# Kernel tuning notes

Measured on AMD Instinct MI355X. Metric: run time of the kernel, lower is better.

Reference implementation:

```python
import jax, jax.numpy as jnp
import numpy as np


def setup_inputs() -> dict:
    key = jax.random.key(0)
    kq, kk, kv = jax.random.split(key, 3)
    B, S, H, D = 2, 2048, 32, 128
    q = jax.random.normal(kq, (B, S, H, D), dtype=jnp.float32)
    k = jax.random.normal(kk, (B, S, H, D), dtype=jnp.float32)
    v = jax.random.normal(kv, (B, S, H, D), dtype=jnp.float32)
    return {"q": q, "k": k, "v": v}


def _causal_attention(q, k, v):
    # q,k,v: [B, S, H, D] (flash-attn layout). Zigzag ring attention computes
    # exactly standard causal attention; zigzag only balances work across ranks.
    B, S, H, D = q.shape
    scale = 1.0 / jnp.sqrt(jnp.asarray(D, q.dtype))
    scores = jnp.einsum('bqhd,bkhd->bhqk', q, k) * scale  # [B,H,S,S]
    causal = jnp.tril(jnp.ones((S, S), dtype=bool))
    scores = jnp.where(causal, scores, jnp.finfo(scores.dtype).min)
    probs = jax.nn.softmax(scores, axis=-1)
    return jnp.einsum('bhqk,bkhd->bqhd', probs, v)  # [B,S,H,D]


def reference(q, k, v):
    out = _causal_attention(q, k, v)
    return jnp.sum(out)
```

## Files before the change

### kernel.cpp

```cpp
#include <hip/hip_runtime.h>
#include <hip/hip_bf16.h>
#include <stdint.h>

#define B_ 2
#define S_ 2048
#define H_ 32
#define D_ 128
#define R_ (B_*H_*S_)
#define PG 2048
#define VSU (B_ * S_)
#define CPB 40

typedef __bf16 bf16x8 __attribute__((ext_vector_type(8)));
typedef float  f32x16 __attribute__((ext_vector_type(16)));

#if __has_builtin(__builtin_amdgcn_exp2f)
#define EXP2F(x) __builtin_amdgcn_exp2f(x)
#else
#define EXP2F(x) exp2f(x)
#endif

#define AS1 __attribute__((address_space(1)))
#define AS3 __attribute__((address_space(3)))

__device__ __forceinline__ unsigned short f2bf(float f) {
  unsigned u = __float_as_uint(f);
  u += 0x7FFFu + ((u >> 16) & 1u);
  return (unsigned short)(u >> 16);
}

__global__ __launch_bounds__(256) void prep(
    const float* __restrict__ k, const float* __restrict__ v,
    unsigned short* __restrict__ kb,
    float* __restrict__ vsum, float* __restrict__ nd, float* __restrict__ out0) {
  const int bid = blockIdx.x;
  const int t = threadIdx.x;
  if (bid == 0 && t == 0) out0[0] = 0.f;

  #pragma unroll
  for (int g = 0; g < (R_ * D_ / 8) / (PG * 256); ++g) {
    const size_t i = (size_t)g * (PG * 256) + bid * 256 + t;
    const float4 a = *reinterpret_cast<const float4*>(k + i * 8);
    const float4 b = *reinterpret_cast<const float4*>(k + i * 8 + 4);
    ushort4 o0, o1;
    o0.x = f2bf(a.x); o0.y = f2bf(a.y); o0.z = f2bf(a.z); o0.w = f2bf(a.w);
    o1.x = f2bf(b.x); o1.y = f2bf(b.y); o1.z = f2bf(b.z); o1.w = f2bf(b.w);
    *reinterpret_cast<ushort4*>(kb + i * 8)     = o0;
    *reinterpret_cast<ushort4*>(kb + i * 8 + 4) = o1;
  }

  #pragma unroll
  for (int g = 0; g < VSU / PG; ++g) {
    const int u = bid + g * PG;
    const int b = u / S_, s = u % S_;
    const int h = t >> 3, i = t & 7;
    const float* p = v + (((size_t)b * S_ + s) * H_ + h) * D_ + i * 16;
    const float4 a0 = *reinterpret_cast<const float4*>(p + 0);
    const float4 a1 = *reinterpret_cast<const float4*>(p + 4);
    const float4 a2 = *reinterpret_cast<const float4*>(p + 8);
    const float4 a3 = *reinterpret_cast<const float4*>(p + 12);
    float sum = (a0.x+a0.y+a0.z+a0.w) + (a1.x+a1.y+a1.z+a1.w)
              + (a2.x+a2.y+a2.z+a2.w) + (a3.x+a3.y+a3.z+a3.w);
    sum += __shfl_xor(sum, 1);
    sum += __shfl_xor(sum, 2);
    sum += __shfl_xor(sum, 4);
    if (i == 0) vsum[((size_t)b * H_ + h) * S_ + s] = sum;
  }

  if (bid < 256) {
    float4* p = reinterpret_cast<float4*>(nd);
    p[(size_t)bid * 256 + t] = float4{0.f, 0.f, 0.f, 0.f};
  }
}

__global__ __launch_bounds__(256, 4) void attn_sum(
    const float* __restrict__ qf_, const unsigned short* __restrict__ kb_,
    const float* __restrict__ vsum, float* __restrict__ numb,
    float* __restrict__ denb) {
  __shared__ uint4 kbuf[4][512];
  __shared__ float vsbuf[4][64];

  const int id = blockIdx.x;
  const int y  = id >> 3;
  const int bh = (id & 7) + 8 * (y / CPB);
  const int c  = y % CPB;

  int qt, h, nch;
  if (c < 4)       { qt = c;                 h = 0;            nch = 1; }
  else if (c < 12) { qt = 4 + ((c - 4) >> 1);  h = (c - 4) & 1;  nch = 2; }
  else if (c < 24) { qt = 8 + (c - 12) / 3;    h = (c - 12) % 3; nch = 3; }
  else             { qt = 12 + ((c - 24) >> 2); h = (c - 24) & 3; nch = 4; }
  const int nkt  = 2 * qt + 2;
  const int bas_ = nkt / nch, rem = nkt % nch;
  const int kt0  = h * bas_ + (h < rem ? h : rem);
  const int kt1  = kt0 + bas_ + (h < rem ? 1 : 0);
  const int st0  = 2 * kt0, st1 = 2 * kt1;

  const int t  = threadIdx.x;
  const int w  = t >> 6;
  const int l  = t & 63;
  const int ln = l & 31, l5 = l >> 5;

  const int b0 = bh >> 5, h0 = bh & 31;
  const int qrow0 = qt * 128 + w * 32;
  const unsigned short* ksrc0 = kb_ + ((size_t)b0 * S_ * H_ + h0) * D_;
  const float* vsrc0 = vsum + (size_t)bh * S_;

  const float sc = 0.0883883476483184f * 1.4426950408889634f;
  bf16x8 qfrag[8];
  {
    const float* qp = qf_ + (((size_t)b0 * S_ + qrow0 + ln) * H_ + h0) * D_ + l5 * 8;
    #pragma unroll
    for (int kb8 = 0; kb8 < 8; ++kb8) {
      const float4 a = *reinterpret_cast<const float4*>(qp + kb8 * 16);
      const float4 b = *reinterpret_cast<const float4*>(qp + kb8 * 16 + 4);
      union { unsigned short u[8]; bf16x8 v; } uu;
      uu.u[0] = f2bf(a.x * sc); uu.u[1] = f2bf(a.y * sc);
      uu.u[2] = f2bf(a.z * sc); uu.u[3] = f2bf(a.w * sc);
      uu.u[4] = f2bf(b.x * sc); uu.u[5] = f2bf(b.y * sc);
      uu.u[6] = f2bf(b.z * sc); uu.u[7] = f2bf(b.w * sc);
      qfrag[kb8] = uu.v;
    }
  }

  auto stage = [&](int st, int slot) {
    #pragma unroll
    for (int j = 0; j < 2; ++j) {
      const int idx = (w * 2 + j) * 64 + l;
      const int r   = idx >> 4;
      const int p   = idx & 15;
      const int cc  = p ^ (r & 15);
      const unsigned short* src = ksrc0 + (size_t)(st * 32 + r) * (H_ * D_) + cc * 8;
      __builtin_amdgcn_global_load_lds(
          (const AS1 void*)src, (AS3 void*)(&kbuf[slot][idx & ~63]), 16, 0, 0);
    }
    __builtin_amdgcn_global_load_lds(
        (const AS1 void*)(vsrc0 + st * 32 + l), (AS3 void*)(&vsbuf[slot][0]), 4, 0, 0);
  };

  float num[16], den[16];
  #pragma unroll
  for (int r = 0; r < 16; ++r) { num[r] = 0.f; den[r] = 0.f; }

  stage(st0, st0 & 3);
  stage(st0 + 1, (st0 + 1) & 3);

  const int xr = ln & 15;
  for (int st = st0; st < st1; ++st) {
    if (st + 1 < st1) asm volatile("s_waitcnt vmcnt(3)" ::: "memory");
    else              asm volatile("s_waitcnt vmcnt(0)" ::: "memory");
    __builtin_amdgcn_s_barrier();
    if (st + 2 < st1) stage(st + 2, (st + 2) & 3);

    const int kbase = st * 32;
    if (kbase <= qrow0 + 31) {
      const int slot = st & 3;
      const uint4* rowb = &kbuf[slot][ln * 16];
      f32x16 sacc = {0.f,0.f,0.f,0.f,0.f,0.f,0.f,0.f,
                     0.f,0.f,0.f,0.f,0.f,0.f,0.f,0.f};
      __builtin_amdgcn_s_setprio(1);
      #pragma unroll
      for (int kb8 = 0; kb8 < 8; ++kb8) {
        const bf16x8 bf = *reinterpret_cast<const bf16x8*>(&rowb[(kb8 * 2 + l5) ^ xr]);
        sacc = __builtin_amdgcn_mfma_f32_32x32x16_bf16(qfrag[kb8], bf, sacc, 0, 0, 0);
      }
      __builtin_amdgcn_s_setprio(0);
      const float vsv = vsbuf[slot][ln];
      if (kbase + 31 <= qrow0) {
        #pragma unroll
        for (int r = 0; r < 16; ++r) {
          const float e = EXP2F(sacc[r]);
          den[r] += e;
          num[r] = fmaf(e, vsv, num[r]);
        }
      } else {
        const int kgc = kbase + ln;
        #pragma unroll
        for (int r = 0; r < 16; ++r) {
          const int qgr = qrow0 + (r & 3) + 8 * (r >> 2) + 4 * l5;
          const float e = (kgc <= qgr) ? EXP2F(sacc[r]) : 0.f;
          den[r] += e;
          num[r] = fmaf(e, vsv, num[r]);
        }
      }
    }
  }

  #pragma unroll
  for (int m = 1; m < 32; m <<= 1) {
    #pragma unroll
    for (int r = 0; r < 16; ++r) {
      num[r] += __shfl_xor(num[r], m);
      den[r] += __shfl_xor(den[r], m);
    }
  }
  if (ln == 0) {
    float* nrow = numb + (size_t)bh * S_;
    float* drow = denb + (size_t)bh * S_;
    #pragma unroll
    for (int r = 0; r < 16; ++r) {
      const int qgr = qrow0 + (r & 3) + 8 * (r >> 2) + 4 * l5;
      atomicAdd(&nrow[qgr], num[r]);
      atomicAdd(&drow[qgr], den[r]);
    }
  }
}

__global__ __launch_bounds__(256) void finalize(
    const float* __restrict__ numb, const float* __restrict__ denb,
    float* __restrict__ out) {
  const int i = blockIdx.x * 256 + threadIdx.x;
  float c = numb[i] / denb[i];
  #pragma unroll
  for (int m = 1; m < 64; m <<= 1) c += __shfl_xor(c, m);
  __shared__ float ps[4];
  if ((threadIdx.x & 63) == 0) ps[threadIdx.x >> 6] = c;
  __syncthreads();
  if (threadIdx.x == 0) atomicAdd(out, ps[0] + ps[1] + ps[2] + ps[3]);
}

extern "C" void kernel_launch(void* const* d_in, const int* in_sizes, int n_in,
                              void* d_out, int out_size, void* d_ws, size_t ws_size,
                              hipStream_t stream) {
  const float* q = (const float*)d_in[0];
  const float* k = (const float*)d_in[1];
  const float* v = (const float*)d_in[2];
  float* out = (float*)d_out;

  unsigned short* kb = (unsigned short*)d_ws;
  float* vsum = (float*)(kb + (size_t)R_ * D_);
  float* numb = vsum + R_;
  float* denb = numb + R_;

  hipLaunchKernelGGL(prep, dim3(PG), dim3(256), 0, stream,
                     k, v, kb, vsum, numb, out);
  hipLaunchKernelGGL(attn_sum, dim3(64 * CPB), dim3(256), 0, stream,
                     q, kb, vsum, numb, denb);
  hipLaunchKernelGGL(finalize, dim3(R_ / 256), dim3(256), 0, stream,
                     numb, denb, out);
}
```

Baseline: 111.5 us.

## Precast Q to bf16 in prep and stage K via registers with software pipeline

The prep kernel now also converts Q to scaled bf16, so the attention kernel loads ready-made bf16 Q fragments instead of converting fp32 Q per block. K staging replaces direct global-to-LDS loads with register loads double-buffered two steps ahead, then swizzled ds_writes to LDS, with adjusted waitcnt accounting. This cuts redundant Q conversion and fp32 Q traffic in the hot kernel. In exchange it adds an extra Q write and read pass in prep plus more register pressure and LDS write instructions in the loop.

Result: slower. 142.0 us (+27.4%).

```diff
diff --git a/kernel.cpp b/kernel.cpp
--- a/kernel.cpp
+++ b/kernel.cpp
@@ -8,7 +8,6 @@
 #define D_ 128
 #define R_ (B_*H_*S_)
 #define PG 2048
-#define VSU (B_ * S_)
 #define CPB 40
 
 typedef __bf16 bf16x8 __attribute__((ext_vector_type(8)));
@@ -30,27 +29,32 @@
 }
 
 __global__ __launch_bounds__(256) void prep(
-    const float* __restrict__ k, const float* __restrict__ v,
-    unsigned short* __restrict__ kb,
+    const float* __restrict__ qf, const float* __restrict__ kf,
+    const float* __restrict__ v,
+    unsigned short* __restrict__ qc, unsigned short* __restrict__ kc,
     float* __restrict__ vsum, float* __restrict__ nd, float* __restrict__ out0) {
   const int bid = blockIdx.x;
   const int t = threadIdx.x;
   if (bid == 0 && t == 0) out0[0] = 0.f;
 
   #pragma unroll
-  for (int g = 0; g < (R_ * D_ / 8) / (PG * 256); ++g) {
-    const size_t i = (size_t)g * (PG * 256) + bid * 256 + t;
-    const float4 a = *reinterpret_cast<const float4*>(k + i * 8);
-    const float4 b = *reinterpret_cast<const float4*>(k + i * 8 + 4);
-    ushort4 o0, o1;
-    o0.x = f2bf(a.x); o0.y = f2bf(a.y); o0.z = f2bf(a.z); o0.w = f2bf(a.w);
-    o1.x = f2bf(b.x); o1.y = f2bf(b.y); o1.z = f2bf(b.z); o1.w = f2bf(b.w);
-    *reinterpret_cast<ushort4*>(kb + i * 8)     = o0;
-    *reinterpret_cast<ushort4*>(kb + i * 8 + 4) = o1;
-  }
-
-  #pragma unroll
-  for (int g = 0; g < VSU / PG; ++g) {
+  for (int g = 0; g < 8; ++g) {
+    const size_t i = (size_t)g * (PG * 256) + (size_t)bid * 256 + t;
+    const float* src; unsigned short* dst; float sc;
+    if (g < 4) { src = qf; dst = qc; sc = 0.0883883476483184f * 1.4426950408889634f; }
+    else       { src = kf - (size_t)R_ * D_; dst = kc - (size_t)R_ * D_; sc = 1.0f; }
+    const float4 a = *reinterpret_cast<const float4*>(src + i * 8);
+    const float4 b = *reinterpret_cast<const float4*>(src + i * 8 + 4);
+    union { unsigned short u[8]; uint4 v4; } o;
+    o.u[0] = f2bf(a.x * sc); o.u[1] = f2bf(a.y * sc);
+    o.u[2] = f2bf(a.z * sc); o.u[3] = f2bf(a.w * sc);
+    o.u[4] = f2bf(b.x * sc); o.u[5] = f2bf(b.y * sc);
+    o.u[6] = f2bf(b.z * sc); o.u[7] = f2bf(b.w * sc);
+    *reinterpret_cast<uint4*>(dst + i * 8) = o.v4;
+  }
+
+  #pragma unroll
+  for (int g = 0; g < (B_ * S_) / PG; ++g) {
     const int u = bid + g * PG;
     const int b = u / S_, s = u % S_;
     const int h = t >> 3, i = t & 7;
@@ -74,7 +78,7 @@
 }
 
 __global__ __launch_bounds__(256, 4) void attn_sum(
-    const float* __restrict__ qf_, const unsigned short* __restrict__ kb_,
+    const unsigned short* __restrict__ qc, const unsigned short* __restrict__ kc,
     const float* __restrict__ vsum, float* __restrict__ numb,
     float* __restrict__ denb) {
   __shared__ uint4 kbuf[4][512];
@@ -103,54 +107,67 @@
 
   const int b0 = bh >> 5, h0 = bh & 31;
   const int qrow0 = qt * 128 + w * 32;
-  const unsigned short* ksrc0 = kb_ + ((size_t)b0 * S_ * H_ + h0) * D_;
+  const unsigned short* kc0 = kc + ((size_t)b0 * S_ * H_ + h0) * D_;
   const float* vsrc0 = vsum + (size_t)bh * S_;
 
-  const float sc = 0.0883883476483184f * 1.4426950408889634f;
   bf16x8 qfrag[8];
   {
-    const float* qp = qf_ + (((size_t)b0 * S_ + qrow0 + ln) * H_ + h0) * D_ + l5 * 8;
+    const unsigned short* qp =
+        qc + (((size_t)b0 * S_ + qrow0 + ln) * H_ + h0) * D_ + l5 * 8;
     #pragma unroll
-    for (int kb8 = 0; kb8 < 8; ++kb8) {
-      const float4 a = *reinterpret_cast<const float4*>(qp + kb8 * 16);
-      const float4 b = *reinterpret_cast<const float4*>(qp + kb8 * 16 + 4);
-      union { unsigned short u[8]; bf16x8 v; } uu;
-      uu.u[0] = f2bf(a.x * sc); uu.u[1] = f2bf(a.y * sc);
-      uu.u[2] = f2bf(a.z * sc); uu.u[3] = f2bf(a.w * sc);
-      uu.u[4] = f2bf(b.x * sc); uu.u[5] = f2bf(b.y * sc);
-      uu.u[6] = f2bf(b.z * sc); uu.u[7] = f2bf(b.w * sc);
-      qfrag[kb8] = uu.v;
-    }
-  }
-
-  auto stage = [&](int st, int slot) {
-    #pragma unroll
-    for (int j = 0; j < 2; ++j) {
-      const int idx = (w * 2 + j) * 64 + l;
-      const int r   = idx >> 4;
-      const int p   = idx & 15;
-      const int cc  = p ^ (r & 15);
-      const unsigned short* src = ksrc0 + (size_t)(st * 32 + r) * (H_ * D_) + cc * 8;
-      __builtin_amdgcn_global_load_lds(
-          (const AS1 void*)src, (AS3 void*)(&kbuf[slot][idx & ~63]), 16, 0, 0);
-    }
+    for (int kb8 = 0; kb8 < 8; ++kb8)
+      qfrag[kb8] = *reinterpret_cast<const bf16x8*>(qp + kb8 * 16);
+  }
+
+  const int rloc = w * 8 + (l >> 3);
+  const int cc1  = (l & 7) * 2;
+  const int xrw  = rloc & 15;
+
+  auto LOADK = [&](int st, uint4& r0, uint4& r1) {
+    const unsigned short* p = kc0 + (size_t)(st * 32 + rloc) * (H_ * D_) + cc1 * 8;
+    r0 = *reinterpret_cast<const uint4*>(p);
+    r1 = *reinterpret_cast<const uint4*>(p + 8);
+  };
+  auto DSW = [&](int slot, uint4 r0, uint4 r1) {
+    kbuf[slot][rloc * 16 + (cc1 ^ xrw)]       = r0;
+    kbuf[slot][rloc * 16 + ((cc1 + 1) ^ xrw)] = r1;
+  };
+  auto VSD = [&](int st) {
     __builtin_amdgcn_global_load_lds(
-        (const AS1 void*)(vsrc0 + st * 32 + l), (AS3 void*)(&vsbuf[slot][0]), 4, 0, 0);
+        (const AS1 void*)(vsrc0 + st * 32 + l),
+        (AS3 void*)(&vsbuf[st & 3][0]), 4, 0, 0);
   };
 
   float num[16], den[16];
   #pragma unroll
   for (int r = 0; r < 16; ++r) { num[r] = 0.f; den[r] = 0.f; }
 
-  stage(st0, st0 & 3);
-  stage(st0 + 1, (st0 + 1) & 3);
+  uint4 a0, a1, b0r, b1r;
+
+  if ((st0 & 1) == 0) LOADK(st0, a0, a1); else LOADK(st0, b0r, b1r);
+  VSD(st0);
+  if (st0 + 1 < st1) {
+    if (((st0 + 1) & 1) == 0) LOADK(st0 + 1, a0, a1); else LOADK(st0 + 1, b0r, b1r);
+    VSD(st0 + 1);
+  }
+  if ((st0 & 1) == 0) DSW(st0 & 3, a0, a1); else DSW(st0 & 3, b0r, b1r);
 
   const int xr = ln & 15;
   for (int st = st0; st < st1; ++st) {
-    if (st + 1 < st1) asm volatile("s_waitcnt vmcnt(3)" ::: "memory");
-    else              asm volatile("s_waitcnt vmcnt(0)" ::: "memory");
+    asm volatile("s_waitcnt lgkmcnt(0)" ::: "memory");
     __builtin_amdgcn_s_barrier();
-    if (st + 2 < st1) stage(st + 2, (st + 2) & 3);
+    if (st + 1 < st1) {
+      if (((st + 1) & 1) == 0) DSW((st + 1) & 3, a0, a1);
+      else                     DSW((st + 1) & 3, b0r, b1r);
+    }
+    if (st + 2 < st1) {
+      if (((st + 2) & 1) == 0) LOADK(st + 2, a0, a1);
+      else                     LOADK(st + 2, b0r, b1r);
+      VSD(st + 2);
+    }
+    if (st + 2 < st1)      asm volatile("s_waitcnt vmcnt(6)" ::: "memory");
+    else if (st + 1 < st1) asm volatile("s_waitcnt vmcnt(3)" ::: "memory");
+    else                   asm volatile("s_waitcnt vmcnt(0)" ::: "memory");
 
     const int kbase = st * 32;
     if (kbase <= qrow0 + 31) {
@@ -227,15 +244,16 @@
   const float* v = (const float*)d_in[2];
   float* out = (float*)d_out;
 
-  unsigned short* kb = (unsigned short*)d_ws;
-  float* vsum = (float*)(kb + (size_t)R_ * D_);
+  unsigned short* qc = (unsigned short*)d_ws;
+  unsigned short* kc = qc + (size_t)R_ * D_;
+  float* vsum = (float*)(kc + (size_t)R_ * D_);
   float* numb = vsum + R_;
   float* denb = numb + R_;
 
   hipLaunchKernelGGL(prep, dim3(PG), dim3(256), 0, stream,
-                     k, v, kb, vsum, numb, out);
+                     q, k, v, qc, kc, vsum, numb, out);
   hipLaunchKernelGGL(attn_sum, dim3(64 * CPB), dim3(256), 0, stream,
-                     q, kb, vsum, numb, denb);
+                     qc, kc, vsum, numb, denb);
   hipLaunchKernelGGL(finalize, dim3(R_ / 256), dim3(256), 0, stream,
                      numb, denb, out);
 }
```

## Fuse K bf16 conversion into attention via register-staged pipeline

Applied to the files above, without the earlier changes.

Removes the separate K fp32-to-bf16 conversion pass from the prep kernel. The attention kernel now loads fp32 K tiles into registers, keeping three stages in flight, and converts them with packed bf16 conversion instructions. It then writes them into swizzled LDS, replacing the async global-to-LDS loads. This saves a full write and reread of a bf16 K copy, but each tile now reads twice as many bytes of fp32 K, register pressure rises, and occupancy drops to 3 blocks per SIMD.

After: 233.3 us. 109% more time.

```diff
diff --git a/kernel.cpp b/kernel.cpp
--- a/kernel.cpp
+++ b/kernel.cpp
@@ -8,7 +8,6 @@
 #define D_ 128
 #define R_ (B_*H_*S_)
 #define PG 2048
-#define VSU (B_ * S_)
 #define CPB 40
 
 typedef __bf16 bf16x8 __attribute__((ext_vector_type(8)));
@@ -23,34 +22,21 @@
 #define AS1 __attribute__((address_space(1)))
 #define AS3 __attribute__((address_space(3)))
 
-__device__ __forceinline__ unsigned short f2bf(float f) {
-  unsigned u = __float_as_uint(f);
-  u += 0x7FFFu + ((u >> 16) & 1u);
-  return (unsigned short)(u >> 16);
+__device__ __forceinline__ unsigned int cvtpk(float a, float b) {
+  unsigned int r;
+  asm volatile("v_cvt_pk_bf16_f32 %0, %1, %2" : "=v"(r) : "v"(a), "v"(b));
+  return r;
 }
 
 __global__ __launch_bounds__(256) void prep(
-    const float* __restrict__ k, const float* __restrict__ v,
-    unsigned short* __restrict__ kb,
-    float* __restrict__ vsum, float* __restrict__ nd, float* __restrict__ out0) {
+    const float* __restrict__ v, float* __restrict__ vsum,
+    float* __restrict__ nd, float* __restrict__ out0) {
   const int bid = blockIdx.x;
   const int t = threadIdx.x;
   if (bid == 0 && t == 0) out0[0] = 0.f;
 
   #pragma unroll
-  for (int g = 0; g < (R_ * D_ / 8) / (PG * 256); ++g) {
-    const size_t i = (size_t)g * (PG * 256) + bid * 256 + t;
-    const float4 a = *reinterpret_cast<const float4*>(k + i * 8);
-    const float4 b = *reinterpret_cast<const float4*>(k + i * 8 + 4);
-    ushort4 o0, o1;
-    o0.x = f2bf(a.x); o0.y = f2bf(a.y); o0.z = f2bf(a.z); o0.w = f2bf(a.w);
-    o1.x = f2bf(b.x); o1.y = f2bf(b.y); o1.z = f2bf(b.z); o1.w = f2bf(b.w);
-    *reinterpret_cast<ushort4*>(kb + i * 8)     = o0;
-    *reinterpret_cast<ushort4*>(kb + i * 8 + 4) = o1;
-  }
-
-  #pragma unroll
-  for (int g = 0; g < VSU / PG; ++g) {
+  for (int g = 0; g < (B_ * S_) / PG; ++g) {
     const int u = bid + g * PG;
     const int b = u / S_, s = u % S_;
     const int h = t >> 3, i = t & 7;
@@ -73,8 +59,8 @@
   }
 }
 
-__global__ __launch_bounds__(256, 4) void attn_sum(
-    const float* __restrict__ qf_, const unsigned short* __restrict__ kb_,
+__global__ __launch_bounds__(256, 3) void attn_sum(
+    const float* __restrict__ qf, const float* __restrict__ kf,
     const float* __restrict__ vsum, float* __restrict__ numb,
     float* __restrict__ denb) {
   __shared__ uint4 kbuf[4][512];
@@ -103,54 +89,81 @@
 
   const int b0 = bh >> 5, h0 = bh & 31;
   const int qrow0 = qt * 128 + w * 32;
-  const unsigned short* ksrc0 = kb_ + ((size_t)b0 * S_ * H_ + h0) * D_;
+  const float* kf0 = kf + ((size_t)b0 * S_ * H_ + h0) * D_;
   const float* vsrc0 = vsum + (size_t)bh * S_;
 
   const float sc = 0.0883883476483184f * 1.4426950408889634f;
   bf16x8 qfrag[8];
   {
-    const float* qp = qf_ + (((size_t)b0 * S_ + qrow0 + ln) * H_ + h0) * D_ + l5 * 8;
+    const float* qp = qf + (((size_t)b0 * S_ + qrow0 + ln) * H_ + h0) * D_ + l5 * 8;
     #pragma unroll
     for (int kb8 = 0; kb8 < 8; ++kb8) {
       const float4 a = *reinterpret_cast<const float4*>(qp + kb8 * 16);
       const float4 b = *reinterpret_cast<const float4*>(qp + kb8 * 16 + 4);
-      union { unsigned short u[8]; bf16x8 v; } uu;
-      uu.u[0] = f2bf(a.x * sc); uu.u[1] = f2bf(a.y * sc);
-      uu.u[2] = f2bf(a.z * sc); uu.u[3] = f2bf(a.w * sc);
-      uu.u[4] = f2bf(b.x * sc); uu.u[5] = f2bf(b.y * sc);
-      uu.u[6] = f2bf(b.z * sc); uu.u[7] = f2bf(b.w * sc);
-      qfrag[kb8] = uu.v;
-    }
-  }
-
-  auto stage = [&](int st, int slot) {
-    #pragma unroll
-    for (int j = 0; j < 2; ++j) {
-      const int idx = (w * 2 + j) * 64 + l;
-      const int r   = idx >> 4;
-      const int p   = idx & 15;
-      const int cc  = p ^ (r & 15);
-      const unsigned short* src = ksrc0 + (size_t)(st * 32 + r) * (H_ * D_) + cc * 8;
-      __builtin_amdgcn_global_load_lds(
-          (const AS1 void*)src, (AS3 void*)(&kbuf[slot][idx & ~63]), 16, 0, 0);
-    }
+      union { unsigned int u[4]; bf16x8 v; } o;
+      o.u[0] = cvtpk(a.x * sc, a.y * sc);
+      o.u[1] = cvtpk(a.z * sc, a.w * sc);
+      o.u[2] = cvtpk(b.x * sc, b.y * sc);
+      o.u[3] = cvtpk(b.z * sc, b.w * sc);
+      qfrag[kb8] = o.v;
+    }
+  }
+
+  float4 sA[4], sB[4], sC[4];
+
+  auto LOADK = [&](int st, float4 (&dst)[4]) {
+    #pragma unroll
+    for (int j = 0; j < 4; ++j) {
+      const int pi = j * 256 + t;
+      const int r = pi >> 5, c4 = pi & 31;
+      dst[j] = *reinterpret_cast<const float4*>(
+          kf0 + (size_t)(st * 32 + r) * (H_ * D_) + c4 * 4);
+    }
+  };
+  auto DSW = [&](int st, const float4 (&src)[4]) {
+    char* base = reinterpret_cast<char*>(&kbuf[st & 3][0]);
+    #pragma unroll
+    for (int j = 0; j < 4; ++j) {
+      const int pi = j * 256 + t;
+      const int r = pi >> 5, c4 = pi & 31;
+      const int cc = c4 >> 1, half = c4 & 1;
+      uint2 val;
+      val.x = cvtpk(src[j].x, src[j].y);
+      val.y = cvtpk(src[j].z, src[j].w);
+      *reinterpret_cast<uint2*>(
+          base + r * 256 + ((cc ^ (r & 15)) * 16 + half * 8)) = val;
+    }
+  };
+  auto VSD = [&](int st) {
     __builtin_amdgcn_global_load_lds(
-        (const AS1 void*)(vsrc0 + st * 32 + l), (AS3 void*)(&vsbuf[slot][0]), 4, 0, 0);
+        (const AS1 void*)(vsrc0 + st * 32 + l),
+        (AS3 void*)(&vsbuf[st & 3][0]), 4, 0, 0);
   };
+  #define SET_OF(stx) ((stx) % 3)
+  #define DO_LOADK(stx) { const int m_ = SET_OF(stx); \
+    if (m_ == 0) LOADK(stx, sA); else if (m_ == 1) LOADK(stx, sB); \
+    else LOADK(stx, sC); VSD(stx); }
+  #define DO_DSW(stx) { const int m_ = SET_OF(stx); \
+    if (m_ == 0) DSW(stx, sA); else if (m_ == 1) DSW(stx, sB); \
+    else DSW(stx, sC); }
 
   float num[16], den[16];
   #pragma unroll
   for (int r = 0; r < 16; ++r) { num[r] = 0.f; den[r] = 0.f; }
 
-  stage(st0, st0 & 3);
-  stage(st0 + 1, (st0 + 1) & 3);
+  DO_LOADK(st0);
+  if (st0 + 1 < st1) DO_LOADK(st0 + 1);
+  if (st0 + 2 < st1) DO_LOADK(st0 + 2);
+  DO_DSW(st0);
 
   const int xr = ln & 15;
   for (int st = st0; st < st1; ++st) {
-    if (st + 1 < st1) asm volatile("s_waitcnt vmcnt(3)" ::: "memory");
-    else              asm volatile("s_waitcnt vmcnt(0)" ::: "memory");
+    asm volatile("s_waitcnt lgkmcnt(0)" ::: "memory");
     __builtin_amdgcn_s_barrier();
-    if (st + 2 < st1) stage(st + 2, (st + 2) & 3);
+    asm volatile("" ::: "memory");
+    if (st + 1 < st1) DO_DSW(st + 1);
+    if (st + 3 < st1) DO_LOADK(st + 3);
+    if (st + 1 >= st1) asm volatile("s_waitcnt vmcnt(0)" ::: "memory");
 
     const int kbase = st * 32;
     if (kbase <= qrow0 + 31) {
@@ -227,15 +240,14 @@
   const float* v = (const float*)d_in[2];
   float* out = (float*)d_out;
 
-  unsigned short* kb = (unsigned short*)d_ws;
-  float* vsum = (float*)(kb + (size_t)R_ * D_);
+  float* vsum = (float*)d_ws;
   float* numb = vsum + R_;
   float* denb = numb + R_;
 
   hipLaunchKernelGGL(prep, dim3(PG), dim3(256), 0, stream,
-                     k, v, kb, vsum, numb, out);
+                     v, vsum, numb, out);
   hipLaunchKernelGGL(attn_sum, dim3(64 * CPB), dim3(256), 0, stream,
-                     q, kb, vsum, numb, denb);
+                     q, k, vsum, numb, denb);
   hipLaunchKernelGGL(finalize, dim3(R_ / 256), dim3(256), 0, stream,
                      numb, denb, out);
 }
```
